# Performance work log

Hardware: AMD Instinct MI355X
Metric: run time of the kernel (lower is better)

Reference implementation:

```python
import jax, jax.numpy as jnp
import numpy as np

T, B, IN_DIM, HID = 512, 64, 512, 1024


def setup_inputs() -> dict:
    key = jax.random.key(0)
    ks = jax.random.split(key, 9)
    s_in = 1.0 / np.sqrt(IN_DIM + HID)  # torch Linear default init scale
    inputs = jax.random.normal(ks[0], (T, B, IN_DIM), dtype=jnp.float32)
    def w(k):
        return jax.random.uniform(k, (IN_DIM + HID, HID), jnp.float32, -s_in, s_in)
    def b(k):
        return jax.random.uniform(k, (HID,), jnp.float32, -s_in, s_in)
    return {
        "inputs": inputs,
        "Wf": w(ks[1]), "bf": b(ks[2]),
        "Wi": w(ks[3]), "bi": b(ks[4]),
        "Wg": w(ks[5]), "bg": b(ks[6]),
        "Wo": w(ks[7]), "bo": b(ks[8]),
    }


def _lstm(inputs, Wf, bf, Wi, bi, Wg, bg, Wo, bo):
    # Fuse the 4 gate linears into one GEMM: [in+hid, 4*hid]
    W = jnp.concatenate([Wf, Wi, Wg, Wo], axis=1)
    bias = jnp.concatenate([bf, bi, bg, bo], axis=0)
    batch = inputs.shape[1]
    h0 = jnp.zeros((batch, HID), inputs.dtype)
    c0 = jnp.zeros((batch, HID), inputs.dtype)

    def step(carry, x):
        hx, cx = carry
        combined = jnp.concatenate([x, hx], axis=1)  # [B, in+hid]
        z = combined @ W + bias                       # [B, 4*hid]
        f = jax.nn.sigmoid(z[:, 0 * HID:1 * HID])
        i = jax.nn.sigmoid(z[:, 1 * HID:2 * HID])
        g = jnp.tanh(z[:, 2 * HID:3 * HID])
        o = jax.nn.sigmoid(z[:, 3 * HID:4 * HID])
        cx = f * cx + i * g
        hx = o * jnp.tanh(cx)
        return (hx, cx), hx

    (hx, cx), stacked = jax.lax.scan(step, (h0, c0), inputs)
    return stacked, hx, cx


def reference(inputs, Wf, bf, Wi, bi, Wg, bg, Wo, bo):
    return _lstm(inputs, Wf, bf, Wi, bi, Wg, bg, Wo, bo)
```

## Files before the change

### kernel.cpp

```cpp
#include <hip/hip_runtime.h>
#include <math.h>


namespace {

constexpr int T_STEPS = 512;
constexpr int B = 64;
constexpr int IN = 512;
constexpr int H = 1024;
constexpr int K = IN + H;
constexpr int NBLK = 256;
constexpr int NXMF = IN / 32;
constexpr int NHMF = H / 32;
constexpr int WPITCH = K + 8;
constexpr int HPITCH = H + 8;

constexpr size_t HBUF_OFF = 0;
constexpr size_t XBUF_OFF = HBUF_OFF + 2ull * B * H * 2;
constexpr size_t BAR_OFF = XBUF_OFF + 2ull * B * IN * 2;
constexpr size_t COMBX_OFF = BAR_OFF + 1056ull * 4;
constexpr size_t NEED_PRE = COMBX_OFF + (size_t)T_STEPS * B * IN * 2;

typedef __attribute__((ext_vector_type(8))) _Float16 f16x8;
typedef __attribute__((ext_vector_type(4))) float f32x4;

__device__ __forceinline__ f16x8 load_sc1_16B(const _Float16* p) {
  union {
    unsigned long long u[2];
    f16x8 v;
  } cv;
  const unsigned long long* q = (const unsigned long long*)p;
  cv.u[0] = __hip_atomic_load(q, __ATOMIC_RELAXED, __HIP_MEMORY_SCOPE_AGENT);
  cv.u[1] =
      __hip_atomic_load(q + 1, __ATOMIC_RELAXED, __HIP_MEMORY_SCOPE_AGENT);
  return cv.v;
}

__device__ __forceinline__ void store_sc1_u64(_Float16* p,
                                              unsigned long long v) {
  __hip_atomic_store((unsigned long long*)p, v, __ATOMIC_RELAXED,
                     __HIP_MEMORY_SCOPE_AGENT);
}

__device__ __forceinline__ void store_sc1_u32(unsigned* p, unsigned v) {
  __hip_atomic_store(p, v, __ATOMIC_RELAXED, __HIP_MEMORY_SCOPE_AGENT);
}

__device__ __forceinline__ float fast_sigmoid(float z) {
  return __builtin_amdgcn_rcpf(1.0f + __expf(-z));
}
__device__ __forceinline__ float fast_tanh(float z) {
  return 1.0f - 2.0f * __builtin_amdgcn_rcpf(1.0f + __expf(2.0f * z));
}

__global__ void prep_pre(const float* __restrict__ x,
                         _Float16* __restrict__ combx,
                         _Float16* __restrict__ hbuf,
                         unsigned* __restrict__ bar) {
  const size_t i = (size_t)blockIdx.x * 256 + threadIdx.x;
  if (i < (size_t)T_STEPS * B * IN) combx[i] = (_Float16)x[i];
  if (i < 2ull * B * H) hbuf[i] = (_Float16)0.f;
  if (i < 1056) bar[i] = 0u;
}

__global__ void prep_fb(const float* __restrict__ x,
                        _Float16* __restrict__ xbuf,
                        _Float16* __restrict__ hbuf,
                        unsigned* __restrict__ bar) {
  const size_t i = (size_t)blockIdx.x * 256 + threadIdx.x;
  if (i < (size_t)B * IN) xbuf[i] = (_Float16)x[i];
  if (i < 2ull * B * H) hbuf[i] = (_Float16)0.f;
  if (i < 1056) bar[i] = 0u;
}

template <bool PRE>
__global__ __launch_bounds__(256, 1) void lstm_persist(
    const float* __restrict__ x, const float* __restrict__ Wf,
    const float* __restrict__ Wi, const float* __restrict__ Wg,
    const float* __restrict__ Wo, const float* __restrict__ bf,
    const float* __restrict__ bi_, const float* __restrict__ bg,
    const float* __restrict__ bo, float* __restrict__ out,
    _Float16* __restrict__ combx, _Float16* __restrict__ xbuf,
    _Float16* __restrict__ hbuf, unsigned* __restrict__ bar) {
  __shared__ _Float16 Wlds[16 * WPITCH];
  __shared__ _Float16 Hlds[16 * HPITCH];

  const int blk = blockIdx.x;
  const int tid = threadIdx.x;
  const int bgrp = blk & 3;
  const int jgrp = blk >> 2;
  const int jbase = jgrp * 16;

  const int lane = tid & 63;
  const int wv = tid >> 6;
  const int q = lane >> 4;
  const int n = lane & 15;
  const int gate = n >> 2;
  const int jj = n & 3;
  const int j0w = jbase + wv * 4;
  const int brow0 = bgrp * 16;

  f16x8 Bfrag[NXMF + NHMF];
  {
    const float* wptr[4] = {Wf, Wi, Wg, Wo};
    for (int c = 0; c < 4; ++c) {
#pragma unroll
      for (int g = 0; g < 4; ++g) {
        const float* wsrc = wptr[g];
        for (int it = 0; it < K / 256; ++it) {
          const int k = it * 256 + tid;
          const float4 w = *(const float4*)(wsrc + (size_t)k * H + jbase + c * 4);
          Wlds[(g * 4 + 0) * WPITCH + k] = (_Float16)w.x;
          Wlds[(g * 4 + 1) * WPITCH + k] = (_Float16)w.y;
          Wlds[(g * 4 + 2) * WPITCH + k] = (_Float16)w.z;
          Wlds[(g * 4 + 3) * WPITCH + k] = (_Float16)w.w;
        }
      }
      __syncthreads();
      if (wv == c) {
#pragma unroll
        for (int kk = 0; kk < NXMF + NHMF; ++kk) {
          Bfrag[kk] = *(const f16x8*)(&Wlds[n * WPITCH + kk * 32 + q * 8]);
        }
      }
      __syncthreads();
    }
  }

  const float* bptr[4] = {bf, bi_, bg, bo};
  const float bias_v = bptr[gate][j0w + jj];

  float c_reg[4] = {0.f, 0.f, 0.f, 0.f};

  unsigned* cnt = bar + bgrp * 16;
  unsigned* flagp = bar + 64 + (bgrp * 8 + ((blk >> 3) & 7)) * 16;

  f32x4 acc_x;
  auto xpart = [&](int t) {
    f32x4 a = {bias_v, bias_v, bias_v, bias_v};
    f32x4 b = {0.f, 0.f, 0.f, 0.f};
    if constexpr (PRE) {
      const _Float16* ab =
          combx + (size_t)t * B * IN + (size_t)(brow0 + n) * IN + q * 8;
#pragma unroll
      for (int kk = 0; kk < NXMF; kk += 2) {
        f16x8 f0 = *(const f16x8*)(ab + kk * 32);
        f16x8 f1 = *(const f16x8*)(ab + (kk + 1) * 32);
        a = __builtin_amdgcn_mfma_f32_16x16x32_f16(f0, Bfrag[kk], a, 0, 0, 0);
        b = __builtin_amdgcn_mfma_f32_16x16x32_f16(f1, Bfrag[kk + 1], b, 0, 0,
                                                   0);
      }
    } else {
      const _Float16* ab =
          xbuf + (size_t)(t & 1) * B * IN + (size_t)(brow0 + n) * IN + q * 8;
#pragma unroll
      for (int kk = 0; kk < NXMF; kk += 2) {
        f16x8 f0 = load_sc1_16B(ab + kk * 32);
        f16x8 f1 = load_sc1_16B(ab + (kk + 1) * 32);
        a = __builtin_amdgcn_mfma_f32_16x16x32_f16(f0, Bfrag[kk], a, 0, 0, 0);
        b = __builtin_amdgcn_mfma_f32_16x16x32_f16(f1, Bfrag[kk + 1], b, 0, 0,
                                                   0);
      }
    }
    acc_x = a + b;
  };

  xpart(0);

  for (int t = 0; t < T_STEPS; ++t) {
    const _Float16* hb =
        hbuf + (size_t)(t & 1) * B * H + (size_t)brow0 * H;
    _Float16* hb_next = hbuf + (size_t)((t + 1) & 1) * B * H;

    {
#pragma unroll
      for (int i = 0; i < 8; ++i) {
        const int g2 = tid + i * 256;
        const int row = g2 >> 7;
        const int c16 = g2 & 127;
        f16x8 v = load_sc1_16B(hb + (size_t)row * H + c16 * 8);
        *(f16x8*)(&Hlds[row * HPITCH + c16 * 8]) = v;
      }
    }
    __syncthreads();

    f32x4 a0 = acc_x;
    f32x4 a1 = {0.f, 0.f, 0.f, 0.f};
    f32x4 a2 = {0.f, 0.f, 0.f, 0.f};
    f32x4 a3 = {0.f, 0.f, 0.f, 0.f};
    {
      const _Float16* hl = &Hlds[n * HPITCH + q * 8];
#pragma unroll
      for (int kk = 0; kk < NHMF; kk += 4) {
        f16x8 f0 = *(const f16x8*)(hl + kk * 32);
        f16x8 f1 = *(const f16x8*)(hl + (kk + 1) * 32);
        f16x8 f2 = *(const f16x8*)(hl + (kk + 2) * 32);
        f16x8 f3 = *(const f16x8*)(hl + (kk + 3) * 32);
        a0 = __builtin_amdgcn_mfma_f32_16x16x32_f16(f0, Bfrag[NXMF + kk], a0,
                                                    0, 0, 0);
        a1 = __builtin_amdgcn_mfma_f32_16x16x32_f16(f1, Bfrag[NXMF + kk + 1],
                                                    a1, 0, 0, 0);
        a2 = __builtin_amdgcn_mfma_f32_16x16x32_f16(f2, Bfrag[NXMF + kk + 2],
                                                    a2, 0, 0, 0);
        a3 = __builtin_amdgcn_mfma_f32_16x16x32_f16(f3, Bfrag[NXMF + kk + 3],
                                                    a3, 0, 0, 0);
      }
    }
    const f32x4 acc = (a0 + a1) + (a2 + a3);

    float v[4];
#pragma unroll
    for (int r = 0; r < 4; ++r) {
      const float z = acc[r];
      v[r] = (gate == 2) ? fast_tanh(z) : fast_sigmoid(z);
    }
    float vi[4], vg[4], vo[4];
#pragma unroll
    for (int r = 0; r < 4; ++r) {
      vi[r] = __shfl(v[r], (lane + 4) & 63, 64);
      vg[r] = __shfl(v[r], (lane + 8) & 63, 64);
      vo[r] = __shfl(v[r], (lane + 12) & 63, 64);
    }
    float hv[4];
#pragma unroll
    for (int r = 0; r < 4; ++r) {
      const float c = fmaf(v[r], c_reg[r], vi[r] * vg[r]);
      c_reg[r] = c;
      hv[r] = vo[r] * fast_tanh(c);
    }
    float h1[4], h2[4], h3[4];
#pragma unroll
    for (int r = 0; r < 4; ++r) {
      h1[r] = __shfl(hv[r], (lane + 1) & 63, 64);
      h2[r] = __shfl(hv[r], (lane + 2) & 63, 64);
      h3[r] = __shfl(hv[r], (lane + 3) & 63, 64);
    }
    if (n == 0) {
#pragma unroll
      for (int r = 0; r < 4; ++r) {
        const int b = brow0 + q * 4 + r;
        union {
          _Float16 h[4];
          unsigned long long u;
        } pk;
        pk.h[0] = (_Float16)hv[r];
        pk.h[1] = (_Float16)h1[r];
        pk.h[2] = (_Float16)h2[r];
        pk.h[3] = (_Float16)h3[r];
        store_sc1_u64(hb_next + (size_t)b * H + j0w, pk.u);
      }
    }

    if (!PRE && t + 1 < T_STEPS && tid < 16) {
      _Float16* xn = xbuf + (size_t)((t + 1) & 1) * B * IN;
      const int row = brow0 + (jgrp >> 2);
      const int off = (jgrp & 3) * 128 + tid * 8;
      const float* xs = x + (size_t)(t + 1) * B * IN + (size_t)row * IN + off;
      const float4 x0 = *(const float4*)xs;
      const float4 x1 = *(const float4*)(xs + 4);
      float vals[8] = {x0.x, x0.y, x0.z, x0.w, x1.x, x1.y, x1.z, x1.w};
#pragma unroll
      for (int i = 0; i < 4; ++i) {
        union {
          _Float16 h[2];
          unsigned u;
        } pk;
        pk.h[0] = (_Float16)vals[2 * i];
        pk.h[1] = (_Float16)vals[2 * i + 1];
        store_sc1_u32((unsigned*)(xn + (size_t)row * IN + off + 2 * i), pk.u);
      }
    }

    if (t + 1 < T_STEPS) {
      __syncthreads();
      if (tid == 64) {
        const unsigned a = __hip_atomic_fetch_add(cnt, 1u, __ATOMIC_RELAXED,
                                                  __HIP_MEMORY_SCOPE_AGENT);
        if (a == 64u * (unsigned)(t + 1) - 1u) {
#pragma unroll
          for (int i = 0; i < 8; ++i)
            store_sc1_u32(bar + 64 + (bgrp * 8 + i) * 16, (unsigned)(t + 1));
        }
      }
      if (n == 0) {
#pragma unroll
        for (int r = 0; r < 4; ++r) {
          const int b = brow0 + q * 4 + r;
          const float4 o4 = make_float4(hv[r], h1[r], h2[r], h3[r]);
          *(float4*)(out + (size_t)t * B * H + (size_t)b * H + j0w) = o4;
        }
      }
      if (PRE) xpart(t + 1);
      if (wv == 0) {
        while (__hip_atomic_load(flagp, __ATOMIC_RELAXED,
                                 __HIP_MEMORY_SCOPE_AGENT) <
               (unsigned)(t + 1)) {
          __builtin_amdgcn_s_sleep(1);
        }
      }
      asm volatile("" ::: "memory");
      __builtin_amdgcn_s_barrier();
      asm volatile("" ::: "memory");
      if (!PRE) xpart(t + 1);
    } else {
      float c1[4], c2[4], c3[4];
#pragma unroll
      for (int r = 0; r < 4; ++r) {
        c1[r] = __shfl(c_reg[r], (lane + 1) & 63, 64);
        c2[r] = __shfl(c_reg[r], (lane + 2) & 63, 64);
        c3[r] = __shfl(c_reg[r], (lane + 3) & 63, 64);
      }
      if (n == 0) {
#pragma unroll
        for (int r = 0; r < 4; ++r) {
          const int b = brow0 + q * 4 + r;
          const float4 o4 = make_float4(hv[r], h1[r], h2[r], h3[r]);
          *(float4*)(out + (size_t)t * B * H + (size_t)b * H + j0w) = o4;
          *(float4*)(out + (size_t)T_STEPS * B * H + (size_t)b * H + j0w) =
              o4;
          const float4 c4 = make_float4(c_reg[r], c1[r], c2[r], c3[r]);
          *(float4*)(out + (size_t)T_STEPS * B * H + (size_t)B * H +
                     (size_t)b * H + j0w) = c4;
        }
      }
    }
  }
}

}

extern "C" void kernel_launch(void* const* d_in, const int* in_sizes, int n_in,
                              void* d_out, int out_size, void* d_ws,
                              size_t ws_size, hipStream_t stream) {
  const float* x = (const float*)d_in[0];
  const float* Wf = (const float*)d_in[1];
  const float* bf = (const float*)d_in[2];
  const float* Wi = (const float*)d_in[3];
  const float* bi = (const float*)d_in[4];
  const float* Wg = (const float*)d_in[5];
  const float* bg = (const float*)d_in[6];
  const float* Wo = (const float*)d_in[7];
  const float* bo = (const float*)d_in[8];
  float* out = (float*)d_out;

  char* ws = (char*)d_ws;
  _Float16* hbuf = (_Float16*)(ws + HBUF_OFF);
  _Float16* xbuf = (_Float16*)(ws + XBUF_OFF);
  unsigned* bar = (unsigned*)(ws + BAR_OFF);
  _Float16* combx = (_Float16*)(ws + COMBX_OFF);

  const bool pre = ws_size >= NEED_PRE;

  if (pre) {
    const size_t n = (size_t)T_STEPS * B * IN;
    prep_pre<<<(unsigned)((n + 255) / 256), 256, 0, stream>>>(x, combx, hbuf,
                                                              bar);
    lstm_persist<true><<<NBLK, 256, 0, stream>>>(
        x, Wf, Wi, Wg, Wo, bf, bi, bg, bo, out, combx, xbuf, hbuf, bar);
  } else {
    prep_fb<<<(2 * B * H + 255) / 256, 256, 0, stream>>>(x, xbuf, hbuf, bar);
    lstm_persist<false><<<NBLK, 256, 0, stream>>>(
        x, Wf, Wi, Wg, Wo, bf, bi, bg, bo, out, combx, xbuf, hbuf, bar);
  }
}
```

Baseline: 4.054 ms.

## Replace atomic-counter grid barrier with per-block flags; split hidden-state load in halves

The per-step inter-block barrier used to have each block atomically increment a shared counter, with the last arriver broadcasting release flags. Now each block writes its own step flag, and one wave polls all 64 flags of its batch group at once with a wave-wide all-check. This removes serialized atomics and the extra release-broadcast hop from the critical path of every timestep. Separately, the hidden-state load into LDS is split into two halves, so the MFMAs on the first half can start while the second half is still loading, at the cost of an extra block sync and more registers.

Result: faster. 3.392 ms (-16.3%).

```diff
diff --git a/kernel.cpp b/kernel.cpp
--- a/kernel.cpp
+++ b/kernel.cpp
@@ -109,7 +109,8 @@
         const float* wsrc = wptr[g];
         for (int it = 0; it < K / 256; ++it) {
           const int k = it * 256 + tid;
-          const float4 w = *(const float4*)(wsrc + (size_t)k * H + jbase + c * 4);
+          const float4 w =
+              *(const float4*)(wsrc + (size_t)k * H + jbase + c * 4);
           Wlds[(g * 4 + 0) * WPITCH + k] = (_Float16)w.x;
           Wlds[(g * 4 + 1) * WPITCH + k] = (_Float16)w.y;
           Wlds[(g * 4 + 2) * WPITCH + k] = (_Float16)w.z;
@@ -132,8 +133,7 @@
 
   float c_reg[4] = {0.f, 0.f, 0.f, 0.f};
 
-  unsigned* cnt = bar + bgrp * 16;
-  unsigned* flagp = bar + 64 + (bgrp * 8 + ((blk >> 3) & 7)) * 16;
+  unsigned* flags = bar + bgrp * 64;
 
   f32x4 acc_x;
   auto xpart = [&](int t) {
@@ -168,19 +168,30 @@
   xpart(0);
 
   for (int t = 0; t < T_STEPS; ++t) {
-    const _Float16* hb =
-        hbuf + (size_t)(t & 1) * B * H + (size_t)brow0 * H;
+    const _Float16* hb = hbuf + (size_t)(t & 1) * B * H + (size_t)brow0 * H;
     _Float16* hb_next = hbuf + (size_t)((t + 1) & 1) * B * H;
 
-    {
-#pragma unroll
-      for (int i = 0; i < 8; ++i) {
-        const int g2 = tid + i * 256;
-        const int row = g2 >> 7;
-        const int c16 = g2 & 127;
-        f16x8 v = load_sc1_16B(hb + (size_t)row * H + c16 * 8);
-        *(f16x8*)(&Hlds[row * HPITCH + c16 * 8]) = v;
-      }
+    f16x8 va[4], vb[4];
+#pragma unroll
+    for (int i = 0; i < 4; ++i) {
+      const int g = tid + i * 256;
+      const int row = g >> 6;
+      const int c16 = g & 63;
+      va[i] = load_sc1_16B(hb + (size_t)row * H + c16 * 8);
+    }
+#pragma unroll
+    for (int i = 0; i < 4; ++i) {
+      const int g = tid + i * 256;
+      const int row = g >> 6;
+      const int c16 = g & 63;
+      vb[i] = load_sc1_16B(hb + (size_t)row * H + 512 + c16 * 8);
+    }
+#pragma unroll
+    for (int i = 0; i < 4; ++i) {
+      const int g = tid + i * 256;
+      const int row = g >> 6;
+      const int c16 = g & 63;
+      *(f16x8*)(&Hlds[row * HPITCH + c16 * 8]) = va[i];
     }
     __syncthreads();
 
@@ -191,7 +202,7 @@
     {
       const _Float16* hl = &Hlds[n * HPITCH + q * 8];
 #pragma unroll
-      for (int kk = 0; kk < NHMF; kk += 4) {
+      for (int kk = 0; kk < NHMF / 2; kk += 4) {
         f16x8 f0 = *(const f16x8*)(hl + kk * 32);
         f16x8 f1 = *(const f16x8*)(hl + (kk + 1) * 32);
         f16x8 f2 = *(const f16x8*)(hl + (kk + 2) * 32);
@@ -206,6 +217,32 @@
                                                     a3, 0, 0, 0);
       }
     }
+#pragma unroll
+    for (int i = 0; i < 4; ++i) {
+      const int g = tid + i * 256;
+      const int row = g >> 6;
+      const int c16 = g & 63;
+      *(f16x8*)(&Hlds[row * HPITCH + 512 + c16 * 8]) = vb[i];
+    }
+    __syncthreads();
+    {
+      const _Float16* hl = &Hlds[n * HPITCH + q * 8];
+#pragma unroll
+      for (int kk = NHMF / 2; kk < NHMF; kk += 4) {
+        f16x8 f0 = *(const f16x8*)(hl + kk * 32);
+        f16x8 f1 = *(const f16x8*)(hl + (kk + 1) * 32);
+        f16x8 f2 = *(const f16x8*)(hl + (kk + 2) * 32);
+        f16x8 f3 = *(const f16x8*)(hl + (kk + 3) * 32);
+        a0 = __builtin_amdgcn_mfma_f32_16x16x32_f16(f0, Bfrag[NXMF + kk], a0,
+                                                    0, 0, 0);
+        a1 = __builtin_amdgcn_mfma_f32_16x16x32_f16(f1, Bfrag[NXMF + kk + 1],
+                                                    a1, 0, 0, 0);
+        a2 = __builtin_amdgcn_mfma_f32_16x16x32_f16(f2, Bfrag[NXMF + kk + 2],
+                                                    a2, 0, 0, 0);
+        a3 = __builtin_amdgcn_mfma_f32_16x16x32_f16(f3, Bfrag[NXMF + kk + 3],
+                                                    a3, 0, 0, 0);
+      }
+    }
     const f32x4 acc = (a0 + a1) + (a2 + a3);
 
     float v[4];
@@ -273,15 +310,7 @@
 
     if (t + 1 < T_STEPS) {
       __syncthreads();
-      if (tid == 64) {
-        const unsigned a = __hip_atomic_fetch_add(cnt, 1u, __ATOMIC_RELAXED,
-                                                  __HIP_MEMORY_SCOPE_AGENT);
-        if (a == 64u * (unsigned)(t + 1) - 1u) {
-#pragma unroll
-          for (int i = 0; i < 8; ++i)
-            store_sc1_u32(bar + 64 + (bgrp * 8 + i) * 16, (unsigned)(t + 1));
-        }
-      }
+      if (tid == 0) store_sc1_u32(flags + jgrp, (unsigned)(t + 1));
       if (n == 0) {
 #pragma unroll
         for (int r = 0; r < 4; ++r) {
@@ -292,9 +321,11 @@
       }
       if (PRE) xpart(t + 1);
       if (wv == 0) {
-        while (__hip_atomic_load(flagp, __ATOMIC_RELAXED,
-                                 __HIP_MEMORY_SCOPE_AGENT) <
-               (unsigned)(t + 1)) {
+        const unsigned tgt = (unsigned)(t + 1);
+        for (;;) {
+          const unsigned f = __hip_atomic_load(flags + lane, __ATOMIC_RELAXED,
+                                               __HIP_MEMORY_SCOPE_AGENT);
+          if (__all(f >= tgt)) break;
           __builtin_amdgcn_s_sleep(1);
         }
       }
```
